# Kernel tuning notes

Measured on AMD Instinct MI355X. Metric: run time of the kernel, lower is better.

## Reference

```python
import jax, jax.numpy as jnp
import numpy as np

M = 2048                      # image side (self.M)
INPUT_SHAPE = (362, 362)      # default forward arg; only used for pad sizing
N_ANGLES = 32
THETA = np.linspace(0.0, np.pi, N_ANGLES)  # radians, as the source uses np.cos(angle)


def _dct_mat(N):
    # DCT-II with norm='ortho': C[k, n] = s_k * cos(pi*(n+0.5)*k/N)
    n = np.arange(N)
    C = np.cos(np.pi * (n[None, :] + 0.5) * n[:, None] / N)
    scale = np.full((N, 1), np.sqrt(2.0 / N))
    scale[0, 0] = np.sqrt(1.0 / N)
    return jnp.asarray((C * scale).astype(np.float32))


def _pad_width():
    diagonal = np.sqrt(2) * max(INPUT_SHAPE)
    pad = [int(np.ceil(diagonal - s)) for s in INPUT_SHAPE]
    new_center = [(s + p) // 2 for s, p in zip(INPUT_SHAPE, pad)]
    old_center = [s // 2 for s in INPUT_SHAPE]
    pad_before = [nc - oc for oc, nc in zip(old_center, new_center)]
    return [(pb, p - pb) for pb, p in zip(pad_before, pad)]


def setup_inputs() -> dict:
    key = jax.random.key(0)
    image = jax.random.normal(key, (M, M), dtype=jnp.float32)
    return {"image": image}


def _forward(image):
    # --- 2D DCT-II (ortho), separable: D = C @ x @ C^T ---
    C = _dct_mat(M)
    d = C @ image @ C.T

    # --- pad (widths derived from input_shape as in the source) ---
    padded = jnp.pad(d, _pad_width())          # [P, P], P = 2198
    P = padded.shape[0]
    center = P // 2

    xs = jnp.arange(P, dtype=jnp.float32)
    yy, xx = jnp.meshgrid(xs, xs, indexing='ij')   # output row (y) / col (x) grid
    angles = jnp.asarray(THETA, dtype=jnp.float32)

    def one_angle(carry, ang):
        cos_a = jnp.cos(ang)
        sin_a = jnp.sin(ang)
        # ImageProjectiveTransformV3 maps output (x, y) -> input coords
        x_in = cos_a * xx + sin_a * yy - center * (cos_a + sin_a - 1.0)
        y_in = -sin_a * xx + cos_a * yy - center * (cos_a - sin_a - 1.0)
        x0 = jnp.floor(x_in)
        y0 = jnp.floor(y_in)
        wx = x_in - x0
        wy = y_in - y0
        # fill_mode='WRAP': wrap sample coordinates modulo image size
        x0i = jnp.mod(x0.astype(jnp.int32), P)
        x1i = (x0i + 1) % P
        y0i = jnp.mod(y0.astype(jnp.int32), P)
        y1i = (y0i + 1) % P
        v00 = padded[y0i, x0i]
        v01 = padded[y0i, x1i]
        v10 = padded[y1i, x0i]
        v11 = padded[y1i, x1i]
        rotated = (1.0 - wy) * ((1.0 - wx) * v00 + wx * v01) \
                + wy * ((1.0 - wx) * v10 + wx * v11)
        # radon line: reduce over rows (axis=0)
        return carry, rotated.sum(axis=0)

    _, lines = jax.lax.scan(one_angle, 0, angles)   # [A, P]
    y = lines.T                                     # [P, A] == tf.transpose(A)
    return y / jnp.max(y)


def reference(image):
    return _forward(image)
```

## Files before the change

### kernel.cpp

```cpp
#include <hip/hip_runtime.h>
#include <hip/hip_bf16.h>
#include <math.h>

#define PDIM 2198
#define PDIM2 2252
#define PADB 75
#define NANG 32
#define NLINE (NANG * PDIM)

#define CB 32
#define RW 32
#define NWIN 69
#define TS 48
#define TSTRIDE 52
#define NBUF 3

typedef __attribute__((ext_vector_type(8))) short bf16x8;
typedef __attribute__((ext_vector_type(4))) float f32x4;

template<bool L> struct BoolC { static constexpr bool value = L; };

#define GLOAD_LDS16(g, l)                                              \
    __builtin_amdgcn_global_load_lds(                                  \
        (const __attribute__((address_space(1))) void*)(g),            \
        (__attribute__((address_space(3))) void*)(l), 16, 0, 0)

#if __has_builtin(__builtin_amdgcn_fractf)
#define FRACTF(x) __builtin_amdgcn_fractf(x)
#else
#define FRACTF(x) ((x) - floorf(x))
#endif

__global__ void gen_dct(__hip_bfloat16* __restrict__ C) {
    int idx = blockIdx.x * 256 + threadIdx.x;
    int k = idx >> 11;
    int n = idx & 2047;
    int t = ((2 * n + 1) * k) & 8191;
    float s = sqrtf(((k == 0) ? 1.0f : 2.0f) / 2048.0f);
    C[idx] = __float2bfloat16(s * cospif((float)t * (1.0f / 4096.0f)));
}

__global__ void cvt_img(const float* __restrict__ in, __hip_bfloat16* __restrict__ out) {
    int i = (blockIdx.x * 256 + threadIdx.x) * 4;
    float4 v = *(const float4*)(in + i);
    out[i + 0] = __float2bfloat16(v.x);
    out[i + 1] = __float2bfloat16(v.y);
    out[i + 2] = __float2bfloat16(v.z);
    out[i + 3] = __float2bfloat16(v.w);
}

__global__ __launch_bounds__(256) void pad_zero(float* __restrict__ padded) {
    int idx = blockIdx.x * 256 + threadIdx.x;
    const int TOPBOT = 2 * PADB * PDIM2;
    if (idx < TOPBOT) {
        int r = idx / PDIM2;
        int c = idx - r * PDIM2;
        int row = (r < PADB) ? r : (2048 + r);
        padded[(size_t)row * PDIM2 + c] = 0.0f;
    } else {
        int i2 = idx - TOPBOT;
        if (i2 >= 2048 * 204) return;
        int rr = i2 / 204;
        int s = i2 - rr * 204;
        int col = (s < PADB) ? s : (2048 + s);
        padded[(size_t)(PADB + rr) * PDIM2 + col] = 0.0f;
    }
}

template<int F32OUT>
__global__ __launch_bounds__(256) void gemm_bt(const __hip_bfloat16* __restrict__ A,
                                               const __hip_bfloat16* __restrict__ B,
                                               void* __restrict__ out,
                                               int ldo, int off) {
    __shared__ __hip_bfloat16 Al[128 * 32];
    __shared__ __hip_bfloat16 Bl[64 * 32];
    const int tid = threadIdx.x;
    const int wid = tid >> 6;
    const int lane = tid & 63;
    const int wr = wid >> 1, wc = wid & 1;
    const int l15 = lane & 15, lhi = lane >> 4;
    const int row0 = blockIdx.y * 128;
    const int col0 = blockIdx.x * 64;

    const __hip_bfloat16* gA = A + (size_t)(row0 + wid * 32 + (lane >> 2)) * 2048 + (lane & 3) * 8;
    const __hip_bfloat16* gB = B + (size_t)(col0 + wid * 16 + (lane >> 2)) * 2048 + (lane & 3) * 8;
    __hip_bfloat16* lA = Al + wid * 1024;
    __hip_bfloat16* lB = Bl + wid * 512;

    f32x4 acc[4][2] = {};

    for (int k0 = 0; k0 < 2048; k0 += 32) {
        GLOAD_LDS16(gA + k0, lA);
        GLOAD_LDS16(gA + 16 * 2048 + k0, lA + 16 * 32);
        GLOAD_LDS16(gB + k0, lB);
        __syncthreads();
        bf16x8 af[4], bfr[2];
#pragma unroll
        for (int m = 0; m < 4; ++m)
            af[m] = *(const bf16x8*)(Al + (wr * 64 + m * 16 + l15) * 32 + lhi * 8);
#pragma unroll
        for (int n = 0; n < 2; ++n)
            bfr[n] = *(const bf16x8*)(Bl + (wc * 32 + n * 16 + l15) * 32 + lhi * 8);
#pragma unroll
        for (int m = 0; m < 4; ++m)
#pragma unroll
            for (int n = 0; n < 2; ++n)
                acc[m][n] = __builtin_amdgcn_mfma_f32_16x16x32_bf16(af[m], bfr[n],
                                                                    acc[m][n], 0, 0, 0);
        __syncthreads();
    }

#pragma unroll
    for (int m = 0; m < 4; ++m) {
        const int row = row0 + wr * 64 + m * 16 + lhi * 4;
#pragma unroll
        for (int n = 0; n < 2; ++n) {
            const int col = col0 + wc * 32 + n * 16 + l15;
            f32x4 v = acc[m][n];
            if (F32OUT) {
                float* p = (float*)out + (size_t)(col + off) * ldo + off + row;
                p[0] = v[0]; p[1] = v[1]; p[2] = v[2]; p[3] = v[3];
            } else {
                __hip_bfloat16* p = (__hip_bfloat16*)out + (size_t)col * 2048 + row;
                p[0] = __float2bfloat16(v[0]);
                p[1] = __float2bfloat16(v[1]);
                p[2] = __float2bfloat16(v[2]);
                p[3] = __float2bfloat16(v[3]);
            }
        }
    }
}

struct AngleArgs {
    float ca[NANG], sa[NANG], ox[NANG], oy[NANG];
};

__global__ __launch_bounds__(256) void radon7(const float* __restrict__ padded,
                                              float* __restrict__ lines,
                                              AngleArgs args) {
    __shared__ float tile[NBUF][TS * TSTRIDE];
    __shared__ float red[4][8];
    const int a = blockIdx.y;
    const int c0 = blockIdx.x * CB;
    const int t = threadIdx.x;
    const int wid = t >> 6, lane = t & 63;
    const int cl = lane >> 3;
    const int rl = lane & 7;
    const int c = c0 + wid * 8 + cl;
    const float ca = args.ca[a], sa = args.sa[a];
    const float ox = args.ox[a], oy = args.oy[a];

    const float cf = (float)c;
    const float xbase = fmaf(ca, cf, ox);
    const float ybase = fmaf(-sa, cf, oy);

    const float xbMin = fminf(fmaf(ca, (float)c0, ox), fmaf(ca, (float)(c0 + CB - 1), ox));
    const float ybMin = fminf(fmaf(-sa, (float)c0, oy), fmaf(-sa, (float)(c0 + CB - 1), oy));
    const bool caPos = (ca >= 0.0f);

    float sum = 0.0f;

    auto origin = [&](int w, int& bx0, int& by0) {
        const float rx = (float)(w * RW);
        const float ry = caPos ? rx : (float)(w * RW + RW - 1);
        bx0 = (int)floorf(fmaf(sa, rx, xbMin)) - 1;
        by0 = (int)floorf(fmaf(ca, ry, ybMin)) - 1;
    };

    auto stage = [&](int buf, int bx0, int by0) {
        int bxs = bx0;
        bxs += (bxs < 0) ? PDIM : 0;
        bxs -= (bxs >= PDIM) ? PDIM : 0;
        const int slab = wid * 12;
#pragma unroll
        for (int iss = 0; iss < 3; ++iss) {
            const int d = iss * 256 + lane * 4;
            if (d < 12 * TSTRIDE) {
                const int rr = d / TSTRIDE;
                const int col = d - rr * TSTRIDE;
                int gy = by0 + slab + rr;
                gy += (gy < 0) ? PDIM : 0;
                gy -= (gy >= PDIM) ? PDIM : 0;
                GLOAD_LDS16(padded + (size_t)gy * PDIM2 + bxs + col,
                            &tile[buf][slab * TSTRIDE + iss * 256]);
            }
        }
    };

    auto computeT = [&](int r0, int buf, int bx0, int by0, auto lastc) {
        const float xbb = xbase - (float)bx0;
        const float ybb = ybase - (float)by0;
        const float* tb = &tile[buf][0];
#pragma unroll
        for (int k = 0; k < 4; ++k) {
            const int r = r0 + rl + 8 * k;
            const float rf = (float)r;
            const float xl = fmaf(sa, rf, xbb);
            const float yl = fmaf(ca, rf, ybb);
            const int xi = (int)xl;
            const int yi = (int)yl;
            const float wx = FRACTF(xl);
            const float wy = FRACTF(yl);
            const float* p = tb + yi * TSTRIDE + xi;
            const float v00 = p[0], v01 = p[1];
            const float v10 = p[TSTRIDE], v11 = p[TSTRIDE + 1];
            const float top = fmaf(wx, v01 - v00, v00);
            const float bot = fmaf(wx, v11 - v10, v10);
            if (!decltype(lastc)::value || r < PDIM) sum = fmaf(wy, bot - top, sum + top);
        }
    };

    int bxr[3], byr[3];
    origin(0, bxr[0], byr[0]);
    stage(0, bxr[0], byr[0]);
    origin(1, bxr[1], byr[1]);
    stage(1, bxr[1], byr[1]);
    for (int w = 0; w < NWIN; ++w) {
        if (w < NWIN - 1) asm volatile("s_waitcnt vmcnt(3)" ::: "memory");
        else              asm volatile("s_waitcnt vmcnt(0)" ::: "memory");
        __builtin_amdgcn_s_barrier();
        __builtin_amdgcn_sched_barrier(0);
        if (w + 2 < NWIN) {
            const int wn = (w + 2) % 3;
            origin(w + 2, bxr[wn], byr[wn]);
            stage(wn, bxr[wn], byr[wn]);
        }
        const int wi = w % 3;
        if (w < NWIN - 1) computeT(w * RW, wi, bxr[wi], byr[wi], BoolC<false>{});
        else              computeT(w * RW, wi, bxr[wi], byr[wi], BoolC<true>{});
    }

    sum += __shfl_xor(sum, 1, 64);
    sum += __shfl_xor(sum, 2, 64);
    sum += __shfl_xor(sum, 4, 64);
    if (rl == 0) red[wid][cl] = sum;
    __syncthreads();
    if (t < 32 && c0 + t < PDIM)
        lines[a * PDIM + c0 + t] = red[t >> 3][t & 7];
}

__global__ __launch_bounds__(256) void max_k(const float* __restrict__ lines,
                                             unsigned int* __restrict__ gmax) {
    const int idx = blockIdx.x * 256 + threadIdx.x;
    float m = (idx < NLINE) ? lines[idx] : -3.4e38f;
#pragma unroll
    for (int off = 32; off > 0; off >>= 1)
        m = fmaxf(m, __shfl_down(m, off, 64));
    __shared__ float wm[4];
    const int lane = threadIdx.x & 63, wid = threadIdx.x >> 6;
    if (lane == 0) wm[wid] = m;
    __syncthreads();
    if (threadIdx.x == 0) {
        float bm = fmaxf(fmaxf(wm[0], wm[1]), fmaxf(wm[2], wm[3]));
        unsigned int b = __float_as_uint(bm);
        unsigned int key = (b & 0x80000000u) ? ~b : (b | 0x80000000u);
        atomicMax(gmax, key);
    }
}

__global__ void norm_k(const float* __restrict__ lines,
                       const unsigned int* __restrict__ gmax,
                       float* __restrict__ out) {
    int idx = blockIdx.x * 256 + threadIdx.x;
    if (idx >= NLINE) return;
    unsigned int u = *gmax;
    unsigned int b = (u & 0x80000000u) ? (u & 0x7fffffffu) : ~u;
    float mx = __uint_as_float(b);
    int c = idx >> 5;
    int a = idx & 31;
    out[idx] = lines[(size_t)a * PDIM + c] / mx;
}

extern "C" void kernel_launch(void* const* d_in, const int* in_sizes, int n_in,
                              void* d_out, int out_size, void* d_ws, size_t ws_size,
                              hipStream_t stream) {
    (void)in_sizes; (void)n_in; (void)out_size; (void)ws_size;
    const float* img = (const float*)d_in[0];
    float* out = (float*)d_out;

    __hip_bfloat16* Cbf   = (__hip_bfloat16*)d_ws;
    __hip_bfloat16* imgbf = Cbf + 4194304;
    __hip_bfloat16* uT    = imgbf + 4194304;
    float* padded  = (float*)(uT + 4194304);
    float* lines   = padded + (size_t)PDIM * PDIM2;
    unsigned int* gmax = (unsigned int*)(lines + NLINE);

    (void)hipMemsetAsync(gmax, 0, sizeof(unsigned int), stream);

    gen_dct<<<16384, 256, 0, stream>>>(Cbf);
    cvt_img<<<4096, 256, 0, stream>>>(img, imgbf);
    pad_zero<<<(2 * PADB * PDIM2 + 2048 * 204 + 255) / 256, 256, 0, stream>>>(padded);

    gemm_bt<0><<<dim3(32, 16), 256, 0, stream>>>(imgbf, Cbf, uT, 2048, 0);
    gemm_bt<1><<<dim3(32, 16), 256, 0, stream>>>(uT, Cbf, padded, PDIM2, PADB);

    AngleArgs aa;
    for (int i = 0; i < NANG; ++i) {
        float th = (float)((double)i * 3.14159265358979323846 / 31.0);
        float ca = (float)cos((double)th);
        float sa = (float)sin((double)th);
        aa.ca[i] = ca;
        aa.sa[i] = sa;
        aa.ox[i] = -1099.0f * (ca + sa - 1.0f);
        aa.oy[i] = -1099.0f * (ca - sa - 1.0f);
    }
    radon7<<<dim3(NWIN, NANG), 256, 0, stream>>>(padded, lines, aa);
    max_k<<<(NLINE + 255) / 256, 256, 0, stream>>>(lines, gmax);
    norm_k<<<(NLINE + 255) / 256, 256, 0, stream>>>(lines, gmax, out);
}
```

Before: 304.6 us.

## Pack padded image as bf16 horizontal pairs so radon reads two LDS words

```diff
diff --git a/kernel.cpp b/kernel.cpp
--- a/kernel.cpp
+++ b/kernel.cpp
@@ -67,6 +67,26 @@
     }
 }
 
+__global__ __launch_bounds__(256) void pack_img(const float* __restrict__ padded,
+                                                unsigned* __restrict__ imgP) {
+    const int W4 = PDIM2 / 4;
+    int idx = blockIdx.x * 256 + threadIdx.x;
+    int y = idx / W4;
+    if (y >= PDIM) return;
+    int x4 = (idx - y * W4) * 4;
+    const float* row = padded + (size_t)y * PDIM2;
+    float4 v = *(const float4*)(row + x4);
+    float v4 = (x4 + 4 < PDIM2) ? row[x4 + 4] : 0.0f;
+    __hip_bfloat162 p0 = __float22bfloat162_rn(make_float2(v.x, v.y));
+    __hip_bfloat162 p1 = __float22bfloat162_rn(make_float2(v.y, v.z));
+    __hip_bfloat162 p2 = __float22bfloat162_rn(make_float2(v.z, v.w));
+    __hip_bfloat162 p3 = __float22bfloat162_rn(make_float2(v.w, v4));
+    uint4 o;
+    o.x = *(unsigned*)&p0; o.y = *(unsigned*)&p1;
+    o.z = *(unsigned*)&p2; o.w = *(unsigned*)&p3;
+    *(uint4*)(imgP + (size_t)y * PDIM2 + x4) = o;
+}
+
 template<int F32OUT>
 __global__ __launch_bounds__(256) void gemm_bt(const __hip_bfloat16* __restrict__ A,
                                                const __hip_bfloat16* __restrict__ B,
@@ -135,10 +155,10 @@
     float ca[NANG], sa[NANG], ox[NANG], oy[NANG];
 };
 
-__global__ __launch_bounds__(256) void radon7(const float* __restrict__ padded,
+__global__ __launch_bounds__(256) void radon8(const unsigned* __restrict__ imgP,
                                               float* __restrict__ lines,
                                               AngleArgs args) {
-    __shared__ float tile[NBUF][TS * TSTRIDE];
+    __shared__ unsigned tile[NBUF][TS * TSTRIDE];
     __shared__ float red[4][8];
     const int a = blockIdx.y;
     const int c0 = blockIdx.x * CB;
@@ -181,7 +201,7 @@
                 int gy = by0 + slab + rr;
                 gy += (gy < 0) ? PDIM : 0;
                 gy -= (gy >= PDIM) ? PDIM : 0;
-                GLOAD_LDS16(padded + (size_t)gy * PDIM2 + bxs + col,
+                GLOAD_LDS16(imgP + (size_t)gy * PDIM2 + bxs + col,
                             &tile[buf][slab * TSTRIDE + iss * 256]);
             }
         }
@@ -190,7 +210,7 @@
     auto computeT = [&](int r0, int buf, int bx0, int by0, auto lastc) {
         const float xbb = xbase - (float)bx0;
         const float ybb = ybase - (float)by0;
-        const float* tb = &tile[buf][0];
+        const unsigned* tb = &tile[buf][0];
 #pragma unroll
         for (int k = 0; k < 4; ++k) {
             const int r = r0 + rl + 8 * k;
@@ -201,9 +221,13 @@
             const int yi = (int)yl;
             const float wx = FRACTF(xl);
             const float wy = FRACTF(yl);
-            const float* p = tb + yi * TSTRIDE + xi;
-            const float v00 = p[0], v01 = p[1];
-            const float v10 = p[TSTRIDE], v11 = p[TSTRIDE + 1];
+            const int idx = yi * TSTRIDE + xi;
+            const unsigned u0 = tb[idx];
+            const unsigned u1 = tb[idx + TSTRIDE];
+            const float v00 = __uint_as_float(u0 << 16);
+            const float v01 = __uint_as_float(u0 & 0xffff0000u);
+            const float v10 = __uint_as_float(u1 << 16);
+            const float v11 = __uint_as_float(u1 & 0xffff0000u);
             const float top = fmaf(wx, v01 - v00, v00);
             const float bot = fmaf(wx, v11 - v10, v10);
             if (!decltype(lastc)::value || r < PDIM) sum = fmaf(wy, bot - top, sum + top);
@@ -281,6 +305,7 @@
     __hip_bfloat16* Cbf   = (__hip_bfloat16*)d_ws;
     __hip_bfloat16* imgbf = Cbf + 4194304;
     __hip_bfloat16* uT    = imgbf + 4194304;
+    unsigned* imgP = (unsigned*)d_ws;
     float* padded  = (float*)(uT + 4194304);
     float* lines   = padded + (size_t)PDIM * PDIM2;
     unsigned int* gmax = (unsigned int*)(lines + NLINE);
@@ -293,6 +318,8 @@
 
     gemm_bt<0><<<dim3(32, 16), 256, 0, stream>>>(imgbf, Cbf, uT, 2048, 0);
     gemm_bt<1><<<dim3(32, 16), 256, 0, stream>>>(uT, Cbf, padded, PDIM2, PADB);
+
+    pack_img<<<(PDIM * (PDIM2 / 4) + 255) / 256, 256, 0, stream>>>(padded, imgP);
 
     AngleArgs aa;
     for (int i = 0; i < NANG; ++i) {
@@ -304,7 +331,7 @@
         aa.ox[i] = -1099.0f * (ca + sa - 1.0f);
         aa.oy[i] = -1099.0f * (ca - sa - 1.0f);
     }
-    radon7<<<dim3(NWIN, NANG), 256, 0, stream>>>(padded, lines, aa);
+    radon8<<<dim3(NWIN, NANG), 256, 0, stream>>>(imgP, lines, aa);
     max_k<<<(NLINE + 255) / 256, 256, 0, stream>>>(lines, gmax);
     norm_k<<<(NLINE + 255) / 256, 256, 0, stream>>>(lines, gmax, out);
 }
```

After: 318.2 us. 1.04x slower.

## Split radon row windows across two blocks and swizzle block-to-angle mapping

Applied to the files above, without the earlier changes.

```diff
diff --git a/kernel.cpp b/kernel.cpp
--- a/kernel.cpp
+++ b/kernel.cpp
@@ -11,6 +11,7 @@
 #define CB 32
 #define RW 32
 #define NWIN 69
+#define WSPLIT 35
 #define TS 48
 #define TSTRIDE 52
 #define NBUF 3
@@ -135,13 +136,20 @@
     float ca[NANG], sa[NANG], ox[NANG], oy[NANG];
 };
 
-__global__ __launch_bounds__(256) void radon7(const float* __restrict__ padded,
-                                              float* __restrict__ lines,
+__global__ __launch_bounds__(256) void radon9(const float* __restrict__ padded,
+                                              float* __restrict__ lines2,
                                               AngleArgs args) {
     __shared__ float tile[NBUF][TS * TSTRIDE];
     __shared__ float red[4][8];
-    const int a = blockIdx.y;
-    const int c0 = blockIdx.x * CB;
+    const int lid = blockIdx.x;
+    const int g = lid >> 3;
+    const int a = (lid & 7) + 8 * (g / 138);
+    const int rem = g % 138;
+    const int rc = rem / 69;
+    const int c0 = (rem % 69) * CB;
+    const int wbeg = rc ? WSPLIT : 0;
+    const int wend = rc ? NWIN : WSPLIT;
+
     const int t = threadIdx.x;
     const int wid = t >> 6, lane = t & 63;
     const int cl = lane >> 3;
@@ -211,16 +219,16 @@
     };
 
     int bxr[3], byr[3];
-    origin(0, bxr[0], byr[0]);
-    stage(0, bxr[0], byr[0]);
-    origin(1, bxr[1], byr[1]);
-    stage(1, bxr[1], byr[1]);
-    for (int w = 0; w < NWIN; ++w) {
-        if (w < NWIN - 1) asm volatile("s_waitcnt vmcnt(3)" ::: "memory");
+    origin(wbeg, bxr[wbeg % 3], byr[wbeg % 3]);
+    stage(wbeg % 3, bxr[wbeg % 3], byr[wbeg % 3]);
+    origin(wbeg + 1, bxr[(wbeg + 1) % 3], byr[(wbeg + 1) % 3]);
+    stage((wbeg + 1) % 3, bxr[(wbeg + 1) % 3], byr[(wbeg + 1) % 3]);
+    for (int w = wbeg; w < wend; ++w) {
+        if (w < wend - 1) asm volatile("s_waitcnt vmcnt(3)" ::: "memory");
         else              asm volatile("s_waitcnt vmcnt(0)" ::: "memory");
         __builtin_amdgcn_s_barrier();
         __builtin_amdgcn_sched_barrier(0);
-        if (w + 2 < NWIN) {
+        if (w + 2 < wend) {
             const int wn = (w + 2) % 3;
             origin(w + 2, bxr[wn], byr[wn]);
             stage(wn, bxr[wn], byr[wn]);
@@ -236,13 +244,19 @@
     if (rl == 0) red[wid][cl] = sum;
     __syncthreads();
     if (t < 32 && c0 + t < PDIM)
-        lines[a * PDIM + c0 + t] = red[t >> 3][t & 7];
-}
-
-__global__ __launch_bounds__(256) void max_k(const float* __restrict__ lines,
-                                             unsigned int* __restrict__ gmax) {
+        lines2[(size_t)rc * NLINE + a * PDIM + c0 + t] = red[t >> 3][t & 7];
+}
+
+__global__ __launch_bounds__(256) void reduce_max_k(const float* __restrict__ lines2,
+                                                    float* __restrict__ lines,
+                                                    unsigned int* __restrict__ gmax) {
     const int idx = blockIdx.x * 256 + threadIdx.x;
-    float m = (idx < NLINE) ? lines[idx] : -3.4e38f;
+    float s = -3.4e38f;
+    if (idx < NLINE) {
+        s = lines2[idx] + lines2[NLINE + idx];
+        lines[idx] = s;
+    }
+    float m = s;
 #pragma unroll
     for (int off = 32; off > 0; off >>= 1)
         m = fmaxf(m, __shfl_down(m, off, 64));
@@ -282,7 +296,8 @@
     __hip_bfloat16* imgbf = Cbf + 4194304;
     __hip_bfloat16* uT    = imgbf + 4194304;
     float* padded  = (float*)(uT + 4194304);
-    float* lines   = padded + (size_t)PDIM * PDIM2;
+    float* lines2  = padded + (size_t)PDIM * PDIM2;
+    float* lines   = lines2 + 2 * (size_t)NLINE;
     unsigned int* gmax = (unsigned int*)(lines + NLINE);
 
     (void)hipMemsetAsync(gmax, 0, sizeof(unsigned int), stream);
@@ -304,7 +319,7 @@
         aa.ox[i] = -1099.0f * (ca + sa - 1.0f);
         aa.oy[i] = -1099.0f * (ca - sa - 1.0f);
     }
-    radon7<<<dim3(NWIN, NANG), 256, 0, stream>>>(padded, lines, aa);
-    max_k<<<(NLINE + 255) / 256, 256, 0, stream>>>(lines, gmax);
+    radon9<<<69 * 2 * NANG, 256, 0, stream>>>(padded, lines2, aa);
+    reduce_max_k<<<(NLINE + 255) / 256, 256, 0, stream>>>(lines2, lines, gmax);
     norm_k<<<(NLINE + 255) / 256, 256, 0, stream>>>(lines, gmax, out);
 }
```

Measured after the change: 314.8 us. +3.3%, slower.
